# Optimization experiments

Measured on AMD Instinct MI355X. Metric: run time of the kernel, lower is better.

The kernel has to match this reference:

```python
import jax, jax.numpy as jnp
import numpy as np

B, E, F, Q = 16, 2048, 8192, 20
D, WD = 256, 300
NUM_ENTITY, NUM_WORD, NUM_RELATION = 100000, 50000, 600
NUM_LAYER = 3
PAGERANK_LAMBDA = 0.8
FACT_SCALE = 3.0
VERY_NEG = -100000000000.0
VERY_SMALL = 1e-10


def setup_inputs() -> dict:
    key = jax.random.key(0)
    ks = jax.random.split(key, 40)
    s = 0.05
    L = NUM_LAYER
    inp = {
        'local_entity': jax.random.randint(ks[0], (B, E), 0, NUM_ENTITY),
        'q2e_adj_mat': jax.random.uniform(ks[1], (B, E, 1), jnp.float32),
        'kb_fact_rel': jax.random.randint(ks[2], (B, F), 0, NUM_RELATION),
        'query_text': jax.random.randint(ks[3], (B, Q), 0, NUM_WORD),
        'answer_dist': jax.random.uniform(ks[4], (B, E), jnp.float32),
        'e2f_ent': jax.random.randint(ks[5], (B, F), 0, E),
        'f2e_ent': jax.random.randint(ks[6], (B, F), 0, E),
        'word_emb': jax.random.normal(ks[7], (NUM_WORD + 1, WD)) * s,
        'entity_emb': jax.random.normal(ks[8], (NUM_ENTITY + 1, WD)) * s,
        'relation_emb': jax.random.normal(ks[9], (NUM_RELATION + 1, 2 * WD)) * s,
        'entity_lin_w': jax.random.normal(ks[10], (D, WD)) * s,
        'entity_lin_b': jnp.zeros((D,)),
        'relation_lin_w': jax.random.normal(ks[11], (D, 2 * WD)) * s,
        'relation_lin_b': jnp.zeros((D,)),
        'lstm_w_ih': jax.random.normal(ks[12], (4 * D, WD)) * s,
        'lstm_w_hh': jax.random.normal(ks[13], (4 * D, D)) * s,
        'lstm_b_ih': jnp.zeros((4 * D,)),
        'lstm_b_hh': jnp.zeros((4 * D,)),
        'q2e_w': jax.random.normal(ks[14], (L, D, D)) * s,
        'q2e_b': jnp.zeros((L, D)),
        'e2q_w': jax.random.normal(ks[15], (L, D, 3 * D)) * s,
        'e2q_b': jnp.zeros((L, D)),
        'e2e_w': jax.random.normal(ks[16], (L, D, 3 * D)) * s,
        'e2e_b': jnp.zeros((L, D)),
        'kb_head_w': jax.random.normal(ks[17], (L, D, D)) * s,
        'kb_head_b': jnp.zeros((L, D)),
        'kb_tail_w': jax.random.normal(ks[18], (L, D, D)) * s,
        'kb_tail_b': jnp.zeros((L, D)),
        'kb_self_w': jax.random.normal(ks[19], (L, D, D)) * s,
        'kb_self_b': jnp.zeros((L, D)),
        'score_w': jax.random.normal(ks[20], (1, D)) * s,
        'score_b': jnp.zeros((1,)),
    }
    return inp


def _lstm(x, w_ih, w_hh, b_ih, b_hh):
    # torch LSTM, single layer, unidirectional, zero init state; gates (i,f,g,o)
    gx = jnp.einsum('btd,gd->btg', x, w_ih) + b_ih + b_hh  # [B,T,4H]
    H = w_hh.shape[1]
    init = (jnp.zeros((x.shape[0], H), x.dtype), jnp.zeros((x.shape[0], H), x.dtype))
    def step(carry, g):
        h, c = carry
        z = g + h @ w_hh.T
        i, f, gg, o = jnp.split(z, 4, axis=-1)
        c = jax.nn.sigmoid(f) * c + jax.nn.sigmoid(i) * jnp.tanh(gg)
        h = jax.nn.sigmoid(o) * jnp.tanh(c)
        return (h, c), h
    (h, _), hs = jax.lax.scan(step, init, jnp.swapaxes(gx, 0, 1))
    return jnp.swapaxes(hs, 0, 1), h  # [B,T,H], [B,H]


def _forward(local_entity, q2e_adj_mat, kb_fact_rel, query_text, e2f_ent, f2e_ent,
             word_emb, entity_emb, relation_emb,
             entity_lin_w, entity_lin_b, relation_lin_w, relation_lin_b,
             lstm_w_ih, lstm_w_hh, lstm_b_ih, lstm_b_hh,
             q2e_w, q2e_b, e2q_w, e2q_b, e2e_w, e2e_b,
             kb_head_w, kb_head_b, kb_tail_w, kb_tail_b, kb_self_w, kb_self_b,
             score_w, score_b):
    bidx = jnp.arange(B)[:, None]
    ent_mask = (local_entity != NUM_ENTITY).astype(jnp.float32)  # [B,E]
    q_mask = (query_text != NUM_WORD).astype(jnp.float32)        # [B,Q]

    # query LSTM encoding (dropout = identity in eval)
    qh, qlast = _lstm(word_emb[query_text], lstm_w_ih, lstm_w_hh, lstm_b_ih, lstm_b_hh)
    query_node = qlast[:, None, :]                               # [B,1,D]

    # fact embeddings
    lf = relation_emb[kb_fact_rel] @ relation_lin_w.T + relation_lin_b  # [B,F,D]
    div = jnp.sqrt(jnp.float32(D))

    # fact <-> query attention
    sim = jnp.einsum('bqd,bfd->bqf', qh, lf) / div
    sim = jax.nn.softmax(sim + (1.0 - q_mask)[:, :, None] * VERY_NEG, axis=1)
    att = jnp.einsum('bqf,bqd->bfd', sim, qh)
    Wf = jnp.sum(att * lf, axis=2) / div                          # [B,F]
    W_tilde = jnp.exp(Wf - jnp.max(Wf, axis=1, keepdims=True))    # [B,F]

    # e2f softmax normalizer: scatter-add fact weights onto head entities
    e2f_softmax = jnp.zeros((B, E), W_tilde.dtype).at[bidx, e2f_ent].add(W_tilde)
    e2f_softmax = jnp.maximum(e2f_softmax, VERY_SMALL)

    # entity embeddings (word_dim != entity_dim -> linear projection)
    le = entity_emb[local_entity] @ entity_lin_w.T + entity_lin_b  # [B,E,D]
    pagerank = q2e_adj_mat[..., 0]                                 # [B,E]

    for i in range(NUM_LAYER):
        q2e = jnp.broadcast_to(query_node @ q2e_w[i].T + q2e_b[i], (B, E, D))
        # fact update: self + gathered head-entity messages
        fact_self = lf @ kb_self_w[i].T + kb_self_b[i]
        head = le @ kb_head_w[i].T + kb_head_b[i]
        e2f_emb = jax.nn.relu(fact_self + jnp.take_along_axis(head, e2f_ent[:, :, None], axis=1))
        norm = W_tilde * jnp.take_along_axis(pagerank / e2f_softmax, e2f_ent, axis=1)  # [B,F]
        e2f_emb = e2f_emb * norm[:, :, None]
        # entity update: self + scattered tail messages
        tail = e2f_emb @ kb_tail_w[i].T + kb_tail_b[i]
        ent_self = le @ kb_self_w[i].T + kb_self_b[i]
        f2e_emb = jax.nn.relu(ent_self + jnp.zeros((B, E, D), le.dtype).at[bidx, f2e_ent].add(tail))
        pagerank = (PAGERANK_LAMBDA * jnp.zeros((B, E), norm.dtype).at[bidx, f2e_ent].add(norm)
                    + (1.0 - PAGERANK_LAMBDA) * pagerank)
        nxt = jnp.concatenate([le, q2e, FACT_SCALE * f2e_emb], axis=2)  # [B,E,3D]
        query_node = jnp.einsum('be,bed->bd', pagerank, nxt @ e2q_w[i].T + e2q_b[i])[:, None, :]
        le = jax.nn.relu(nxt @ e2e_w[i].T + e2e_b[i])

    score = (le @ score_w.T + score_b)[..., 0]                     # [B,E]
    return score


def reference(local_entity, q2e_adj_mat, kb_fact_rel, query_text, answer_dist,
              e2f_ent, f2e_ent, word_emb, entity_emb, relation_emb,
              entity_lin_w, entity_lin_b, relation_lin_w, relation_lin_b,
              lstm_w_ih, lstm_w_hh, lstm_b_ih, lstm_b_hh,
              q2e_w, q2e_b, e2q_w, e2q_b, e2e_w, e2e_b,
              kb_head_w, kb_head_b, kb_tail_w, kb_tail_b, kb_self_w, kb_self_b,
              score_w, score_b):
    return _forward(local_entity, q2e_adj_mat, kb_fact_rel, query_text, e2f_ent, f2e_ent,
                    word_emb, entity_emb, relation_emb,
                    entity_lin_w, entity_lin_b, relation_lin_w, relation_lin_b,
                    lstm_w_ih, lstm_w_hh, lstm_b_ih, lstm_b_hh,
                    q2e_w, q2e_b, e2q_w, e2q_b, e2e_w, e2e_b,
                    kb_head_w, kb_head_b, kb_tail_w, kb_tail_b, kb_self_w, kb_self_b,
                    score_w, score_b)
```

## Files before the change

kernel.cpp:

```cpp
#include <hip/hip_runtime.h>
#include <hip/hip_bf16.h>

typedef __hip_bfloat16 bf16;
typedef __attribute__((ext_vector_type(8))) short bf16x8;
typedef __attribute__((ext_vector_type(4))) float f32x4;

#define BB 16
#define EE 2048
#define FF 8192
#define QQ 20
#define DD 256
#define WDIM 300
#define NWORD 50000
#define VERY_NEG_F (-1.0e11f)

static __device__ __forceinline__ float b2f(bf16 x){ return __bfloat162float(x); }
static __device__ __forceinline__ bf16 f2b(float x){ return __float2bfloat16(x); }
static __device__ __forceinline__ float sigm(float x){ return 1.f/(1.f+expf(-x)); }
static __device__ __forceinline__ void ld4bf(const bf16* p, float v[4]){
  short4 s = *(const short4*)p;
  v[0]=b2f(*(const bf16*)&s.x); v[1]=b2f(*(const bf16*)&s.y);
  v[2]=b2f(*(const bf16*)&s.z); v[3]=b2f(*(const bf16*)&s.w);
}
static __device__ __forceinline__ void st4bf(bf16* p, float a,float b,float c,float d){
  unsigned short u[4]; bf16 t;
  t=f2b(a);u[0]=*(unsigned short*)&t; t=f2b(b);u[1]=*(unsigned short*)&t;
  t=f2b(c);u[2]=*(unsigned short*)&t; t=f2b(d);u[3]=*(unsigned short*)&t;
  *(short4*)p=*(short4*)u;
}

#define O_GX       0UL
#define O_QH       1310720UL
#define O_QNODE    1638400UL
#define O_RELLIN   1654784UL
#define O_WR       2270208UL
#define O_WMAX     2308864UL
#define O_WT       2309120UL
#define O_E2FS     2833408UL
#define O_PR       2964480UL
#define O_PRAGG    3095552UL
#define O_Q2EV     3226624UL
#define O_Q2EVB    3243008UL
#define O_RELSELF  3251200UL
#define O_NORM     3866624UL
#define O_WNXT     4390912UL
#define O_PRSUM    4440064UL
#define O_CNT      4440320UL
#define O_CUR      4571392UL
#define O_BSTART   4702464UL
#define O_BIDX     4834048UL
#define O_ELWPAD   5358336UL
#define O_FLAG     5522176UL
#define O_CVT      5522432UL
#define O_AGG      10915584UL
#define O_ENTSELF  27692800UL
#define O_LEA      44470016UL
#define O_LEB      61247232UL
#define O_HEAD     78024448UL
#define O_F2EEMB   94801664UL

#define C_ELB   0
#define C_RLW   256
#define C_RLB   153856
#define C_WIH   154112
#define C_WHH   461312
#define C_BIH   723456
#define C_BHH   724480
#define C_Q2EW  725504
#define C_Q2EB  922112
#define C_E2QW  922880
#define C_E2QB  1512704
#define C_E2EW  1513472
#define C_E2EB  2103296
#define C_KHW   2104064
#define C_KHB   2300672
#define C_KTW   2301440
#define C_KTB   2498048
#define C_KSW   2498816
#define C_KSB   2695424
#define C_SCW   2696192
#define C_SCB   2696448

__global__ __launch_bounds__(256) void k_sniff(const unsigned short* ee, int* flag){
  __shared__ int red[256];
  int c=0;
  for(int i=threadIdx.x;i<4096;i+=256){
    int ex=(ee[2*i]>>7)&0xFF;
    c += (ex>=192);
  }
  red[threadIdx.x]=c; __syncthreads();
  for(int o=128;o;o>>=1){ if(threadIdx.x<o) red[threadIdx.x]+=red[threadIdx.x+o]; __syncthreads(); }
  if(!threadIdx.x) flag[0] = (red[0]>64) ? 1 : 0;
}

struct CvtJobs{ const void* src[20]; bf16* dst[20]; int n[20]; int sc[20]; };
__global__ __launch_bounds__(256) void k_cvt(CvtJobs J, const int* dfl){
  const int isf=*dfl;
  int j=blockIdx.y;
  int n=J.n[j];
  int i4=(blockIdx.x*256+threadIdx.x)*4;
  if(i4>=n) return;
  float m = (J.sc[j] && ((i4%768)>=512)) ? 3.f : 1.f;
  bf16* d=J.dst[j]+i4;
  if(isf){
    const float* s=(const float*)J.src[j]+i4;
    if(i4+4<=n){ float4 t=*(const float4*)s; st4bf(d,t.x*m,t.y*m,t.z*m,t.w*m); }
    else for(int r=0;i4+r<n;r++) d[r]=f2b(s[r]*m);
  } else {
    const bf16* s=(const bf16*)J.src[j]+i4;
    if(i4+4<=n){ float v[4]; ld4bf(s,v); st4bf(d,v[0]*m,v[1]*m,v[2]*m,v[3]*m); }
    else for(int r=0;i4+r<n;r++) d[r]=f2b(b2f(s[r])*m);
  }
}

__global__ __launch_bounds__(256) void k_cvtwhh(const void* src, bf16* wf, const int* dfl){
  const int isf=*dfl;
  int fid=blockIdx.x*256+threadIdx.x;
  int lane=fid&63, kt=(fid>>6)&7, gt=fid>>9;
  int l16=lane&15, q=lane>>4;
  long so=(long)(gt*16+l16)*256 + kt*32 + q*8;
  float v[8];
  if(isf){ const float* s=(const float*)src+so;
    #pragma unroll
    for(int j=0;j<8;j++) v[j]=s[j];
  } else { const bf16* s=(const bf16*)src+so; ld4bf(s,v); ld4bf(s+4,v+4); }
  bf16* d=wf+(long)fid*8;
  st4bf(d,v[0],v[1],v[2],v[3]); st4bf(d+4,v[4],v[5],v[6],v[7]);
}

__global__ __launch_bounds__(256) void k_cvtelw(const void* src, bf16* dst, const int* dfl){
  const int isf=*dfl;
  int r=blockIdx.x;
  for(int c=threadIdx.x;c<320;c+=256){
    float v=0.f;
    if(c<300) v = isf ? ((const float*)src)[r*300+c] : b2f(((const bf16*)src)[r*300+c]);
    dst[(long)r*320+c]=f2b(v);
  }
}

__global__ __launch_bounds__(256) void k_cnt(const int* f2e, int* cnt){
  int i=blockIdx.x*256+threadIdx.x;
  atomicAdd(&cnt[((i>>13)<<11)+f2e[i]], 1);
}
__global__ __launch_bounds__(1024) void k_scan(const int* cnt, int* bstart){
  __shared__ int ps[1024];
  int t=threadIdx.x;
  int loc[32]; int s=0;
  #pragma unroll
  for(int j=0;j<32;j++){ loc[j]=s; s+=cnt[t*32+j]; }
  ps[t]=s; __syncthreads();
  for(int off=1;off<1024;off<<=1){
    int v=(t>=off)?ps[t-off]:0;
    __syncthreads(); ps[t]+=v; __syncthreads();
  }
  int base=(t? ps[t-1]:0);
  #pragma unroll
  for(int j=0;j<32;j++) bstart[t*32+j]=base+loc[j];
  if(t==1023) bstart[32768]=ps[1023];
}
__global__ __launch_bounds__(256) void k_fill(const int* f2e, const int* bstart, int* cur, int* bidx){
  int i=blockIdx.x*256+threadIdx.x;
  int key=((i>>13)<<11)+f2e[i];
  int pos=bstart[key]+atomicAdd(&cur[key],1);
  bidx[pos]=i;
}

__global__ __launch_bounds__(256) void k_gx(const int* qtext, const void* wemb,
    const bf16* wih, const bf16* bih, const bf16* bhh, float* gx, const int* dfl,
    int* lcnt){
  if(blockIdx.x==0 && threadIdx.x<32) lcnt[threadIdx.x]=0;
  const int isf=*dfl;
  int bt=blockIdx.x;
  __shared__ float xr[WDIM];
  int w=qtext[bt];
  for(int k4=threadIdx.x*4;k4<WDIM;k4+=1024){
    if(isf){ float4 t=*(const float4*)((const float*)wemb+(long)w*WDIM+k4);
             xr[k4]=t.x;xr[k4+1]=t.y;xr[k4+2]=t.z;xr[k4+3]=t.w; }
    else   { float v[4]; ld4bf((const bf16*)wemb+(long)w*WDIM+k4,v);
             xr[k4]=v[0];xr[k4+1]=v[1];xr[k4+2]=v[2];xr[k4+3]=v[3]; }
  }
  __syncthreads();
  #pragma unroll
  for(int s=0;s<4;s++){
    int g=threadIdx.x+256*s;
    float acc=b2f(bih[g])+b2f(bhh[g]);
    const bf16* wr=wih+(long)g*WDIM;
    for(int k4=0;k4<WDIM;k4+=4){
      float v[4]; ld4bf(wr+k4,v);
      acc+=v[0]*xr[k4]+v[1]*xr[k4+1]+v[2]*xr[k4+2]+v[3]*xr[k4+3];
    }
    gx[bt*1024+g]=acc;
  }
}

#define NLB 8
__global__ __launch_bounds__(512) void k_mega(const float* gx, const bf16* wf,
    float* qh, float* qnode, bf16* hbuf, int* lcnt,
    const void* remb, const bf16* rlw, const bf16* rlb, float* rel_lin,
    const int* local_entity, const void* emb, bf16* A0,
    const void* adj, float* pr, const int* dfl){
  const int bid=blockIdx.x, tid=threadIdx.x;
  if(bid<NLB){
    __shared__ bf16  hlds[16*264];
    __shared__ float zs[4*16*32];
    __shared__ bf16  hsl[512];
    const int k=bid;
    const int wv=tid>>6, lane=tid&63, q=lane>>4, l16=lane&15;
    const int gt=(wv>>1)*16 + k*2 + (wv&1);
    const int b=tid>>5, u=tid&31, gu=k*32+u;
    bf16x8 wreg[8];
    #pragma unroll
    for(int kt=0;kt<8;kt++)
      wreg[kt]=*(const bf16x8*)(wf + (((long)(gt*8+kt))*64 + lane)*8);
    float c=0.f;
    float gxr[4];
    #pragma unroll
    for(int g=0;g<4;g++) gxr[g]=gx[(b*QQ+0)*1024 + g*256 + gu];
    for(int t=0;t<QQ;t++){
      f32x4 acc=(f32x4){0.f,0.f,0.f,0.f};
      if(t){
        while(__hip_atomic_load(lcnt+(t-1), __ATOMIC_RELAXED, __HIP_MEMORY_SCOPE_AGENT) < NLB)
          __builtin_amdgcn_s_sleep(2);
        __builtin_amdgcn_sched_barrier(0);
        const bf16* hb = hbuf + (t&1)*4096;
        {
          int r=tid>>5, cc=(tid&31)*8;
          unsigned long long v0=__hip_atomic_load((const unsigned long long*)(hb + r*256 + cc),
                         __ATOMIC_RELAXED, __HIP_MEMORY_SCOPE_AGENT);
          unsigned long long v1=__hip_atomic_load((const unsigned long long*)(hb + r*256 + cc + 4),
                         __ATOMIC_RELAXED, __HIP_MEMORY_SCOPE_AGENT);
          *(unsigned long long*)&hlds[r*264 + cc] = v0;
          *(unsigned long long*)&hlds[r*264 + cc + 4] = v1;
        }
        __syncthreads();
        #pragma unroll
        for(int kt=0;kt<8;kt++){
          bf16x8 af=*(const bf16x8*)&hlds[l16*264 + kt*32 + q*8];
          acc=__builtin_amdgcn_mfma_f32_16x16x32_bf16(af,wreg[kt],acc,0,0,0);
        }
      }
      #pragma unroll
      for(int r=0;r<4;r++) zs[(wv>>1)*512 + (q*4+r)*32 + (wv&1)*16 + l16]=acc[r];
      __syncthreads();
      float zi=zs[0*512+b*32+u]+gxr[0];
      float zf=zs[1*512+b*32+u]+gxr[1];
      float zg=zs[2*512+b*32+u]+gxr[2];
      float zo=zs[3*512+b*32+u]+gxr[3];
      { int tn=(t<QQ-1)?t+1:t;
        #pragma unroll
        for(int g=0;g<4;g++) gxr[g]=gx[(b*QQ+tn)*1024 + g*256 + gu];
      }
      c=sigm(zf)*c+sigm(zi)*tanhf(zg);
      float hv=sigm(zo)*tanhf(c);
      hsl[tid]=f2b(hv);
      __syncthreads();
      if(t<QQ-1){
        if(tid<128){
          bf16* hw=hbuf + ((t+1)&1)*4096;
          int bb=tid>>3, p=tid&7;
          unsigned long long v=*(unsigned long long*)&hsl[bb*32+p*4];
          __hip_atomic_store((unsigned long long*)(hw + bb*256 + k*32 + p*4), v,
                             __ATOMIC_RELAXED, __HIP_MEMORY_SCOPE_AGENT);
        }
        __syncthreads();
        if(tid==0)
          __hip_atomic_fetch_add(lcnt+t, 1, __ATOMIC_RELAXED, __HIP_MEMORY_SCOPE_AGENT);
      }
      __builtin_nontemporal_store(hv, &qh[(long)(b*QQ+t)*256+gu]);
      if(t==QQ-1) qnode[(b<<8)+gu]=hv;
    }
  } else if(bid<309){
    __shared__ float rr[2][2*WDIM];
    const int isf=*dfl;
    const int half=tid>>8, d=tid&255;
    const int r=(bid-8)*2+half;
    if(r<601){
      for(int k4=d*4;k4<2*WDIM;k4+=1024){
        if(isf){ float4 t4=*(const float4*)((const float*)remb+(long)r*2*WDIM+k4);
                 rr[half][k4]=t4.x;rr[half][k4+1]=t4.y;rr[half][k4+2]=t4.z;rr[half][k4+3]=t4.w; }
        else   { float v[4]; ld4bf((const bf16*)remb+(long)r*2*WDIM+k4,v);
                 rr[half][k4]=v[0];rr[half][k4+1]=v[1];rr[half][k4+2]=v[2];rr[half][k4+3]=v[3]; }
      }
    }
    __syncthreads();
    if(r<601){
      float acc=b2f(rlb[d]);
      const bf16* wr=rlw+(long)d*2*WDIM;
      for(int k4=0;k4<2*WDIM;k4+=4){
        float v[4]; ld4bf(wr+k4,v);
        acc+=v[0]*rr[half][k4]+v[1]*rr[half][k4+1]+v[2]*rr[half][k4+2]+v[3]*rr[half][k4+3];
      }
      rel_lin[r*DD+d]=acc;
    }
  } else if(bid<325){
    const int isf=*dfl;
    int i4=((bid-309)*512+tid)*4;
    if(isf){ *(float4*)(pr+i4)=*(const float4*)((const float*)adj+i4); }
    else { float v[4]; ld4bf((const bf16*)adj+i4,v);
           float4 t; t.x=v[0];t.y=v[1];t.z=v[2];t.w=v[3]; *(float4*)(pr+i4)=t; }
  } else {
    const int isf=*dfl;
    int row=(bid-325)*4+(tid>>7); int t=tid&127;
    int ent=local_entity[row];
    bf16* dst=A0+(long)row*320;
    if(t<75){
      float v[4];
      if(isf){ float4 x=*(const float4*)((const float*)emb+(long)ent*WDIM+t*4);
               v[0]=x.x;v[1]=x.y;v[2]=x.z;v[3]=x.w; }
      else ld4bf((const bf16*)emb+(long)ent*WDIM+t*4, v);
      st4bf(dst+t*4, v[0],v[1],v[2],v[3]);
    } else if(t<80){
      st4bf(dst+t*4, 0.f,0.f,0.f,0.f);
    }
  }
}

__global__ __launch_bounds__(256) void k_simwr(const float* qh, const float* rel_lin,
    const int* qtext, float* Wr){
  int b = blockIdx.x, rc = blockIdx.y;
  __shared__ float qhb[QQ*DD];
  __shared__ float qm[QQ];
  for(int i=threadIdx.x;i<QQ*DD;i+=256) qhb[i]=qh[b*QQ*DD+i];
  if(threadIdx.x<QQ) qm[threadIdx.x] = (qtext[b*QQ+threadIdx.x]!=NWORD)?0.f:VERY_NEG_F;
  __syncthreads();
  int r = rc*256+threadIdx.x;
  if(r>=601) return;
  float s[QQ];
  #pragma unroll
  for(int q=0;q<QQ;q++) s[q]=0.f;
  for(int k=0;k<DD;k++){
    float rl = rel_lin[r*DD+k];
    #pragma unroll
    for(int q=0;q<QQ;q++) s[q] += qhb[q*DD+k]*rl;
  }
  float m=-1e30f;
  #pragma unroll
  for(int q=0;q<QQ;q++){ s[q]*=0.0625f; m=fmaxf(m, s[q]+qm[q]); }
  float sum=0.f, w=0.f;
  #pragma unroll
  for(int q=0;q<QQ;q++){ float p=expf(s[q]+qm[q]-m); sum+=p; w+=p*s[q]; }
  Wr[b*601+r] = w/sum;
}

__global__ __launch_bounds__(256) void k_wmax(const float* Wr, const int* rel, float* wmax,
    float* e2fs){
  int b=blockIdx.x; __shared__ float red[256];
  {
    int g=b*256+threadIdx.x;
    float4 z={0.f,0.f,0.f,0.f};
    *(float4*)(e2fs+g*8)=z; *(float4*)(e2fs+g*8+4)=z;
  }
  float m=-1e30f;
  for(int f=threadIdx.x;f<FF;f+=256) m=fmaxf(m, Wr[b*601+rel[b*FF+f]]);
  red[threadIdx.x]=m; __syncthreads();
  for(int o=128;o;o>>=1){ if(threadIdx.x<o) red[threadIdx.x]=fmaxf(red[threadIdx.x],red[threadIdx.x+o]); __syncthreads(); }
  if(!threadIdx.x) wmax[b]=red[0];
}
__global__ __launch_bounds__(256) void k_wt(const float* Wr, const int* rel,
    const float* wmax, const int* e2f, float* wt, float* e2fs,
    float* pragg, float* wnxtb, float* prsum){
  int i = blockIdx.x*256+threadIdx.x;
  if(i<32768) pragg[i]=0.f;
  if(i<12288) wnxtb[i]=0.f;
  if(i<16)    prsum[i]=0.f;
  int b = i>>13;
  float v = expf(Wr[b*601+rel[i]] - wmax[b]);
  wt[i]=v;
  atomicAdd(e2fs + (b<<11) + e2f[i], v);
}

template<int TK,int CONCAT,int EPI>
static __device__ __forceinline__ void mg_body(const bf16* A, const bf16* W,
    const bf16* bias, bf16* out, const bf16* Aq2, const bf16* Af2,
    const int* cnt, const bf16* addb, int m0, int tid){
  const int lane=tid&63, q=lane>>4, l16=lane&15;
  const int n0=(tid>>6)*64;
  const int bidx_=m0>>11;
  f32x4 acc[4][4];
  #pragma unroll
  for(int i=0;i<4;i++)
    #pragma unroll
    for(int j=0;j<4;j++) acc[i][j]=(f32x4){0.f,0.f,0.f,0.f};
  #pragma unroll
  for(int k0=0;k0<TK;k0+=32){
    int kk=k0+q*8;
    bf16x8 af[4], bw[4];
    #pragma unroll
    for(int mi=0;mi<4;mi++){
      int row=m0+mi*16+l16;
      const bf16* ap;
      if(CONCAT){
        if(kk<256)      ap=A  +(long)row*256+kk;
        else if(kk<512) ap=Aq2+(bidx_<<8)+(kk-256);
        else            ap=Af2+(long)row*256+(kk-512);
      } else ap=A+(long)row*TK+kk;
      af[mi]=*(const bf16x8*)ap;
    }
    #pragma unroll
    for(int ni=0;ni<4;ni++)
      bw[ni]=*(const bf16x8*)(W+(long)(n0+ni*16+l16)*TK+kk);
    #pragma unroll
    for(int mi=0;mi<4;mi++)
      #pragma unroll
      for(int ni=0;ni<4;ni++)
        acc[mi][ni]=__builtin_amdgcn_mfma_f32_16x16x32_bf16(af[mi],bw[ni],acc[mi][ni],0,0,0);
  }
  #pragma unroll
  for(int ni=0;ni<4;ni++){
    int col=n0+ni*16+l16;
    float bv=b2f(bias[col]);
    #pragma unroll
    for(int mi=0;mi<4;mi++){
      #pragma unroll
      for(int r=0;r<4;r++){
        int row=m0+mi*16+q*4+r;
        float v=acc[mi][ni][r];
        if(EPI==0) v+=bv;
        else if(EPI==1) v=fmaxf(v+bv,0.f);
        else {
          v += (float)cnt[row]*bv + b2f(addb[(long)row*256+col]);
          v=fmaxf(v,0.f);
        }
        out[(long)row*256+col]=f2b(v);
      }
    }
  }
}

struct MG {
  const bf16* A; const bf16* W; const bf16* bias; bf16* out;
  const bf16* Aq2; const bf16* Af2;
  const int* cnt; const bf16* addb;
};
template<int CONCAT,int EPI,int TK>
__global__ __launch_bounds__(256) void k_mgemm(MG p){
  mg_body<TK,CONCAT,EPI>(p.A,p.W,p.bias,p.out,p.Aq2,p.Af2,p.cnt,p.addb,
                         blockIdx.x*64,threadIdx.x);
}

struct L1 {
  const float* rel_lin; const bf16* ksw; const bf16* ksb;
  const float* qnode; const bf16* q2ew; const bf16* q2eb;
  float* relself; float* q2ev; bf16* q2evb;
  const bf16* A; const bf16* khw; const bf16* khb; bf16* headb; bf16* entself;
  const float* wt; const float* pr; const float* e2fs;
  const int* e2f; const int* f2e; float* normv; float* pragg;
};
__global__ __launch_bounds__(256) void k_lay1(L1 p){
  const int bid=blockIdx.x, tid=threadIdx.x;
  if(bid<617){
    __shared__ float xr[DD];
    int d=tid;
    if(bid<601){
      xr[d]=p.rel_lin[bid*DD+d]; __syncthreads();
      float acc=b2f(p.ksb[d]);
      const bf16* wr=p.ksw+(long)d*DD;
      for(int k4=0;k4<DD;k4+=4){
        float v[4]; ld4bf(wr+k4,v);
        acc+=v[0]*xr[k4]+v[1]*xr[k4+1]+v[2]*xr[k4+2]+v[3]*xr[k4+3];
      }
      p.relself[bid*DD+d]=acc;
    } else {
      int b=bid-601;
      xr[d]=p.qnode[(b<<8)+d]; __syncthreads();
      float acc=b2f(p.q2eb[d]);
      const bf16* wr=p.q2ew+(long)d*DD;
      for(int k4=0;k4<DD;k4+=4){
        float v[4]; ld4bf(wr+k4,v);
        acc+=v[0]*xr[k4]+v[1]*xr[k4+1]+v[2]*xr[k4+2]+v[3]*xr[k4+3];
      }
      p.q2ev[(b<<8)+d]=acc;
      p.q2evb[(b<<8)+d]=f2b(acc);
    }
  } else if(bid<1641){
    int g=bid-617;
    int m0=(g&511)*64;
    if(g<512) mg_body<256,0,0>(p.A,p.khw,p.khb,p.headb,0,0,0,0,m0,tid);
    else      mg_body<256,0,0>(p.A,p.ksw,p.ksb,p.entself,0,0,0,0,m0,tid);
  } else {
    int i=(bid-1641)*256+tid;
    int b=i>>13;
    int e=p.e2f[i];
    float v=p.wt[i]*p.pr[(b<<11)+e]/fmaxf(p.e2fs[(b<<11)+e],1e-10f);
    p.normv[i]=v;
    atomicAdd(p.pragg+(b<<11)+p.f2e[i], v);
  }
}

__global__ __launch_bounds__(256) void k_agg(const int* bstart, const int* bidx,
    const int* rel, const int* e2f, const float* normv, const float* relself,
    const bf16* head, bf16* agg){
  int eidx=blockIdx.x*4+(threadIdx.x>>6);
  int lane=threadIdx.x&63;
  int b=eidx>>11;
  float a0=0.f,a1=0.f,a2=0.f,a3=0.f;
  int s=bstart[eidx], e=bstart[eidx+1];
  for(int i=s;i<e;i++){
    int f=bidx[i];
    int r=rel[f]; int ent=e2f[f]; float nv=normv[f];
    float4 rs=*(const float4*)&relself[r*DD+lane*4];
    float hd[4]; ld4bf(head+(long)(((b<<11)+ent)*DD+lane*4),hd);
    a0+=fmaxf(rs.x+hd[0],0.f)*nv; a1+=fmaxf(rs.y+hd[1],0.f)*nv;
    a2+=fmaxf(rs.z+hd[2],0.f)*nv; a3+=fmaxf(rs.w+hd[3],0.f)*nv;
  }
  st4bf(agg+(long)eidx*DD+lane*4, a0,a1,a2,a3);
}

__global__ __launch_bounds__(256) void k_wnxt(const float* praggc, float* pragg, float* pr,
    const bf16* le, const bf16* f2e, float* wnxt, float* prsum){
  __shared__ float r1[4*256];
  __shared__ float r3[4*256];
  __shared__ float rp[4];
  const int b=blockIdx.x, ch=blockIdx.y;
  const int wv=threadIdx.x>>6, lane=threadIdx.x&63;
  const int pe0=(b<<11)+ch*64+wv*16;
  float pv=0.f;
  if(lane<16){
    int pe=pe0+lane;
    pv=0.8f*praggc[pe]+0.2f*pr[pe];
    pr[pe]=pv;
    pragg[pe]=0.f;
  }
  float a1[4]={0.f,0.f,0.f,0.f}, a3[4]={0.f,0.f,0.f,0.f}, ap=0.f;
  #pragma unroll
  for(int r=0;r<16;r++){
    float p=__shfl(pv, r, 64);
    long base=((long)(pe0+r))<<8;
    float v1[4],v3[4];
    ld4bf(le +base+lane*4, v1);
    ld4bf(f2e+base+lane*4, v3);
    #pragma unroll
    for(int j=0;j<4;j++){ a1[j]+=p*v1[j]; a3[j]+=p*v3[j]; }
    ap+=p;
  }
  #pragma unroll
  for(int j=0;j<4;j++){ r1[wv*256+lane*4+j]=a1[j]; r3[wv*256+lane*4+j]=a3[j]; }
  if(!lane) rp[wv]=ap;
  __syncthreads();
  const int t=threadIdx.x;
  float s1=r1[t]+r1[256+t]+r1[512+t]+r1[768+t];
  float s3=r3[t]+r3[256+t]+r3[512+t]+r3[768+t];
  atomicAdd(&wnxt[b*768+t], s1);
  atomicAdd(&wnxt[b*768+512+t], s3);
  if(!t) atomicAdd(&prsum[b], rp[0]+rp[1]+rp[2]+rp[3]);
}

__global__ __launch_bounds__(256) void k_e2eq(MG p, const float* q2ev,
    const bf16* qw, const bf16* qb, float* wnxtb, float* prsum, float* qnode){
  if(blockIdx.x<512){
    mg_body<768,1,1>(p.A,p.W,p.bias,p.out,p.Aq2,p.Af2,0,0,blockIdx.x*64,threadIdx.x);
  } else {
    int b=blockIdx.x-512, d=threadIdx.x;
    __shared__ float xr[768];
    float ps=prsum[b];
    xr[d]=wnxtb[b*768+d];            wnxtb[b*768+d]=0.f;
    xr[256+d]=ps*q2ev[(b<<8)+d];
    xr[512+d]=wnxtb[b*768+512+d];    wnxtb[b*768+512+d]=0.f;
    __syncthreads();
    if(d==0) prsum[b]=0.f;
    float acc=0.f;
    const bf16* wr=qw+(long)d*768;
    for(int k4=0;k4<768;k4+=4){
      float v[4]; ld4bf(wr+k4,v);
      acc+=v[0]*xr[k4]+v[1]*xr[k4+1]+v[2]*xr[k4+2]+v[3]*xr[k4+3];
    }
    qnode[(b<<8)+d]=acc+ps*b2f(qb[d]);
  }
}

__global__ __launch_bounds__(256) void k_score(const bf16* le, const bf16* sw,
    const bf16* sb, void* out, const int* dfl){
  const int isf=*dfl;
  int o=blockIdx.x*4 + (threadIdx.x>>6);
  int lane=threadIdx.x&63;
  float v[4],wv[4];
  ld4bf(le+(long)o*DD+lane*4,v); ld4bf(sw+lane*4,wv);
  float acc=v[0]*wv[0]+v[1]*wv[1]+v[2]*wv[2]+v[3]*wv[3];
  for(int off=32;off;off>>=1) acc+=__shfl_down(acc,off,64);
  if(!lane){
    float r=acc+b2f(sb[0]);
    if(isf) ((float*)out)[o]=r; else ((bf16*)out)[o]=f2b(r);
  }
}

extern "C" void kernel_launch(void* const* d_in, const int* in_sizes, int n_in,
                              void* d_out, int out_size, void* d_ws, size_t ws_size,
                              hipStream_t stream){
  const int*  local_entity=(const int*)d_in[0];
  const void* q2e_adj     =d_in[1];
  const int*  kb_fact_rel =(const int*)d_in[2];
  const int*  query_text  =(const int*)d_in[3];
  const int*  e2f_ent     =(const int*)d_in[5];
  const int*  f2e_ent     =(const int*)d_in[6];
  const void* word_emb    =d_in[7];
  const void* entity_emb  =d_in[8];
  const void* relation_emb=d_in[9];

  char* ws=(char*)d_ws;
  float* gx      =(float*)(ws+O_GX);
  float* qh      =(float*)(ws+O_QH);
  float* qnode   =(float*)(ws+O_QNODE);
  float* rel_lin =(float*)(ws+O_RELLIN);
  float* Wr      =(float*)(ws+O_WR);
  float* wmax    =(float*)(ws+O_WMAX);
  float* wt      =(float*)(ws+O_WT);
  float* e2fs    =(float*)(ws+O_E2FS);
  float* pr      =(float*)(ws+O_PR);
  float* pragg   =(float*)(ws+O_PRAGG);
  float* q2ev    =(float*)(ws+O_Q2EV);
  bf16*  q2evb   =(bf16*)(ws+O_Q2EVB);
  float* relself =(float*)(ws+O_RELSELF);
  float* normv   =(float*)(ws+O_NORM);
  float* wnxt    =(float*)(ws+O_WNXT);
  float* prsum   =(float*)(ws+O_PRSUM);
  int*   cnt     =(int*)(ws+O_CNT);
  int*   cur     =(int*)(ws+O_CUR);
  int*   bstart  =(int*)(ws+O_BSTART);
  int*   bidx    =(int*)(ws+O_BIDX);
  bf16*  elwpad  =(bf16*)(ws+O_ELWPAD);
  int*   dflag   =(int*)(ws+O_FLAG);
  bf16*  cw      =(bf16*)(ws+O_CVT);
  bf16*  agg     =(bf16*)(ws+O_AGG);
  bf16*  A0      =(bf16*)(ws+O_AGG);
  bf16*  entself =(bf16*)(ws+O_ENTSELF);
  bf16*  leA     =(bf16*)(ws+O_LEA);
  bf16*  leB     =(bf16*)(ws+O_LEB);
  bf16*  headb   =(bf16*)(ws+O_HEAD);
  bf16*  f2eemb  =(bf16*)(ws+O_F2EEMB);
  bf16*  hbuf    =(bf16*)(ws+O_LEA);
  int*   lcnt    =(int*)(ws+O_LEA+16384);

  k_sniff<<<1,256,0,stream>>>((const unsigned short*)entity_emb, dflag);

  CvtJobs J;
  int cntj=0;
  auto add=[&](int in_idx, long coff, int n, int sc){
    J.src[cntj]=d_in[in_idx]; J.dst[cntj]=cw+coff; J.n[cntj]=n; J.sc[cntj]=sc; cntj++;
  };
  add(11,C_ELB,256,0);
  add(12,C_RLW,153600,0);  add(13,C_RLB,256,0);
  add(14,C_WIH,307200,0);
  add(16,C_BIH,1024,0);    add(17,C_BHH,1024,0);
  add(18,C_Q2EW,196608,0); add(19,C_Q2EB,768,0);
  add(20,C_E2QW,589824,1); add(21,C_E2QB,768,0);
  add(22,C_E2EW,589824,1); add(23,C_E2EB,768,0);
  add(24,C_KHW,196608,0);  add(25,C_KHB,768,0);
  add(26,C_KTW,196608,0);  add(27,C_KTB,768,0);
  add(28,C_KSW,196608,0);  add(29,C_KSB,768,0);
  add(30,C_SCW,256,0);     add(31,C_SCB,1,0);
  k_cvt<<<dim3(576,20),256,0,stream>>>(J, dflag);
  k_cvtwhh<<<128,256,0,stream>>>(d_in[15], cw+C_WHH, dflag);
  k_cvtelw<<<256,256,0,stream>>>(d_in[10], elwpad, dflag);

  hipMemsetAsync(cnt, 0, (size_t)2*BB*EE*4, stream);
  k_cnt <<<BB*FF/256,256,0,stream>>>(f2e_ent, cnt);
  k_scan<<<1,1024,0,stream>>>(cnt, bstart);
  k_fill<<<BB*FF/256,256,0,stream>>>(f2e_ent, bstart, cur, bidx);

  k_gx   <<<BB*QQ,256,0,stream>>>(query_text, word_emb, cw+C_WIH, cw+C_BIH, cw+C_BHH, gx, dflag, lcnt);
  k_mega<<<8517,512,0,stream>>>(gx, cw+C_WHH, qh, qnode, hbuf, lcnt,
      relation_emb, cw+C_RLW, cw+C_RLB, rel_lin,
      local_entity, entity_emb, A0,
      q2e_adj, pr, dflag);
  k_simwr<<<dim3(BB,3),256,0,stream>>>(qh, rel_lin, query_text, Wr);
  k_wmax <<<BB,256,0,stream>>>(Wr, kb_fact_rel, wmax, e2fs);
  k_wt   <<<BB*FF/256,256,0,stream>>>(Wr, kb_fact_rel, wmax, e2f_ent, wt, e2fs,
                                      pragg, wnxt, prsum);

  {
    MG p{}; p.A=A0; p.W=elwpad; p.bias=cw+C_ELB; p.out=leA;
    k_mgemm<0,0,320><<<BB*EE/64,256,0,stream>>>(p);
  }

  bf16* le_cur=leA; bf16* le_nxt=leB;
  for(int i=0;i<3;i++){
    {
      L1 p{};
      p.rel_lin=rel_lin; p.ksw=cw+C_KSW+(long)i*65536; p.ksb=cw+C_KSB+(long)i*256;
      p.qnode=qnode; p.q2ew=cw+C_Q2EW+(long)i*65536; p.q2eb=cw+C_Q2EB+(long)i*256;
      p.relself=relself; p.q2ev=q2ev; p.q2evb=q2evb;
      p.A=le_cur; p.khw=cw+C_KHW+(long)i*65536; p.khb=cw+C_KHB+(long)i*256;
      p.headb=headb; p.entself=entself;
      p.wt=wt; p.pr=pr; p.e2fs=e2fs;
      p.e2f=e2f_ent; p.f2e=f2e_ent; p.normv=normv; p.pragg=pragg;
      k_lay1<<<2153,256,0,stream>>>(p);
    }
    k_agg <<<BB*EE/4,256,0,stream>>>(bstart, bidx, kb_fact_rel, e2f_ent, normv, relself, headb, agg);
    {
      MG p{}; p.A=agg; p.W=cw+C_KTW+(long)i*65536; p.bias=cw+C_KTB+(long)i*256;
      p.out=f2eemb; p.cnt=cnt; p.addb=entself;
      k_mgemm<0,2,256><<<BB*EE/64,256,0,stream>>>(p);
    }
    k_wnxt <<<dim3(BB,32),256,0,stream>>>(pragg, pragg, pr, le_cur, f2eemb, wnxt, prsum);
    {
      MG p{}; p.A=le_cur; p.W=cw+C_E2EW+(long)i*196608; p.bias=cw+C_E2EB+(long)i*256;
      p.out=le_nxt; p.Aq2=q2evb; p.Af2=f2eemb;
      k_e2eq<<<512+BB,256,0,stream>>>(p, q2ev,
          cw+C_E2QW+(long)i*196608, cw+C_E2QB+(long)i*256, wnxt, prsum, qnode);
    }
    bf16* t=le_cur; le_cur=le_nxt; le_nxt=t;
  }

  k_score<<<BB*EE/4,256,0,stream>>>(le_cur, cw+C_SCW, cw+C_SCB, d_out, dflag);
}
```

Before: 979.2 us.

## Stage GEMM A tiles into LDS via async global_load_lds with 128-row blocks

Rewrites the layer GEMMs (kb_head/kb_self, kb_tail, e2e) to use 512-thread blocks that cover 128 rows. Each block stages its 128x256 bf16 A tile into swizzled LDS with global_load_lds, and the warps then read fragments from LDS. The head and self GEMMs now share one staged tile, and the e2e concat GEMM stages both A operands and broadcasts the per-batch query fragment directly. The aim is to cut redundant global loads of A and improve reuse, at the cost of 64-128KB of LDS per block, which lowers occupancy. The e2e blocks also have to hold two 64KB buffers.

```diff
diff --git a/kernel.cpp b/kernel.cpp
--- a/kernel.cpp
+++ b/kernel.cpp
@@ -4,6 +4,8 @@
 typedef __hip_bfloat16 bf16;
 typedef __attribute__((ext_vector_type(8))) short bf16x8;
 typedef __attribute__((ext_vector_type(4))) float f32x4;
+typedef __attribute__((address_space(1))) const void* gas_t;
+typedef __attribute__((address_space(3))) void* las_t;
 
 #define BB 16
 #define EE 2048
@@ -345,8 +347,7 @@
 __global__ __launch_bounds__(256) void k_wmax(const float* Wr, const int* rel, float* wmax,
     float* e2fs){
   int b=blockIdx.x; __shared__ float red[256];
-  {
-    int g=b*256+threadIdx.x;
+  { int g=b*256+threadIdx.x;
     float4 z={0.f,0.f,0.f,0.f};
     *(float4*)(e2fs+g*8)=z; *(float4*)(e2fs+g*8+4)=z;
   }
@@ -369,13 +370,17 @@
   atomicAdd(e2fs + (b<<11) + e2f[i], v);
 }
 
-template<int TK,int CONCAT,int EPI>
-static __device__ __forceinline__ void mg_body(const bf16* A, const bf16* W,
-    const bf16* bias, bf16* out, const bf16* Aq2, const bf16* Af2,
-    const int* cnt, const bf16* addb, int m0, int tid){
-  const int lane=tid&63, q=lane>>4, l16=lane&15;
-  const int n0=(tid>>6)*64;
-  const int bidx_=m0>>11;
+struct MG {
+  const bf16* A; const bf16* W; const bf16* bias; bf16* out;
+  const bf16* Aq2; const bf16* Af2;
+  const int* cnt; const bf16* addb;
+};
+template<int CONCAT,int EPI,int TK>
+__global__ __launch_bounds__(256) void k_mgemm(MG p){
+  const int m0 = blockIdx.x*64;
+  const int lane = threadIdx.x&63;
+  const int q = lane>>4, l16 = lane&15;
+  const int n0 = (threadIdx.x>>6)*64;
   f32x4 acc[4][4];
   #pragma unroll
   for(int i=0;i<4;i++)
@@ -386,19 +391,65 @@
     int kk=k0+q*8;
     bf16x8 af[4], bw[4];
     #pragma unroll
+    for(int mi=0;mi<4;mi++)
+      af[mi]=*(const bf16x8*)(p.A+(long)(m0+mi*16+l16)*TK+kk);
+    #pragma unroll
+    for(int ni=0;ni<4;ni++)
+      bw[ni]=*(const bf16x8*)(p.W+(long)(n0+ni*16+l16)*TK+kk);
+    #pragma unroll
+    for(int mi=0;mi<4;mi++)
+      #pragma unroll
+      for(int ni=0;ni<4;ni++)
+        acc[mi][ni]=__builtin_amdgcn_mfma_f32_16x16x32_bf16(af[mi],bw[ni],acc[mi][ni],0,0,0);
+  }
+  #pragma unroll
+  for(int ni=0;ni<4;ni++){
+    int col=n0+ni*16+l16;
+    float bv=b2f(p.bias[col]);
+    #pragma unroll
     for(int mi=0;mi<4;mi++){
-      int row=m0+mi*16+l16;
-      const bf16* ap;
-      if(CONCAT){
-        if(kk<256)      ap=A  +(long)row*256+kk;
-        else if(kk<512) ap=Aq2+(bidx_<<8)+(kk-256);
-        else            ap=Af2+(long)row*256+(kk-512);
-      } else ap=A+(long)row*TK+kk;
-      af[mi]=*(const bf16x8*)ap;
-    }
-    #pragma unroll
-    for(int ni=0;ni<4;ni++)
-      bw[ni]=*(const bf16x8*)(W+(long)(n0+ni*16+l16)*TK+kk);
+      #pragma unroll
+      for(int r=0;r<4;r++){
+        int row=m0+mi*16+q*4+r;
+        float v=acc[mi][ni][r]+bv;
+        p.out[(long)row*256+col]=f2b(v);
+      }
+    }
+  }
+}
+
+static __device__ __forceinline__ void stage64(const char* g, char* l, int tid){
+  const int wv=tid>>6, lane=tid&63;
+  #pragma unroll
+  for(int it=0;it<8;++it){
+    int chunk=it*8192+wv*1024;
+    int off=chunk+lane*16;
+    int src=off^(((off>>9)&7)<<4);
+    __builtin_amdgcn_global_load_lds((gas_t)(g+src),(las_t)(l+chunk),16,0,0);
+  }
+}
+static __device__ __forceinline__ bf16x8 lds_a(const char* l, int r, int kk){
+  int b=(r*512+kk*2)^((r&7)<<4);
+  return *(const bf16x8*)(l+b);
+}
+template<int EPI>
+static __device__ __forceinline__ void mg2_k256(const char* ldsA, const bf16* W,
+    const bf16* bias, bf16* out, const int* cnt, const bf16* addb, int m0, int tid){
+  const int lane=tid&63, q=lane>>4, l16=lane&15;
+  const int wv=tid>>6, wr=wv>>2, wc=wv&3, n0=wc*64;
+  f32x4 acc[4][4];
+  #pragma unroll
+  for(int i=0;i<4;i++)
+    #pragma unroll
+    for(int j=0;j<4;j++) acc[i][j]=(f32x4){0.f,0.f,0.f,0.f};
+  #pragma unroll
+  for(int k0=0;k0<256;k0+=32){
+    int kk=k0+q*8;
+    bf16x8 af[4], bw[4];
+    #pragma unroll
+    for(int mi=0;mi<4;mi++) af[mi]=lds_a(ldsA, wr*64+mi*16+l16, kk);
+    #pragma unroll
+    for(int ni=0;ni<4;ni++) bw[ni]=*(const bf16x8*)(W+(long)(n0+ni*16+l16)*256+kk);
     #pragma unroll
     for(int mi=0;mi<4;mi++)
       #pragma unroll
@@ -413,7 +464,7 @@
     for(int mi=0;mi<4;mi++){
       #pragma unroll
       for(int r=0;r<4;r++){
-        int row=m0+mi*16+q*4+r;
+        int row=m0+wr*64+mi*16+q*4+r;
         float v=acc[mi][ni][r];
         if(EPI==0) v+=bv;
         else if(EPI==1) v=fmaxf(v+bv,0.f);
@@ -427,17 +478,6 @@
   }
 }
 
-struct MG {
-  const bf16* A; const bf16* W; const bf16* bias; bf16* out;
-  const bf16* Aq2; const bf16* Af2;
-  const int* cnt; const bf16* addb;
-};
-template<int CONCAT,int EPI,int TK>
-__global__ __launch_bounds__(256) void k_mgemm(MG p){
-  mg_body<TK,CONCAT,EPI>(p.A,p.W,p.bias,p.out,p.Aq2,p.Af2,p.cnt,p.addb,
-                         blockIdx.x*64,threadIdx.x);
-}
-
 struct L1 {
   const float* rel_lin; const bf16* ksw; const bf16* ksb;
   const float* qnode; const bf16* q2ew; const bf16* q2eb;
@@ -446,45 +486,60 @@
   const float* wt; const float* pr; const float* e2fs;
   const int* e2f; const int* f2e; float* normv; float* pragg;
 };
-__global__ __launch_bounds__(256) void k_lay1(L1 p){
+__global__ __launch_bounds__(512) void k_lay1(L1 p){
+  __shared__ char smem[65536];
   const int bid=blockIdx.x, tid=threadIdx.x;
   if(bid<617){
-    __shared__ float xr[DD];
-    int d=tid;
-    if(bid<601){
-      xr[d]=p.rel_lin[bid*DD+d]; __syncthreads();
-      float acc=b2f(p.ksb[d]);
-      const bf16* wr=p.ksw+(long)d*DD;
-      for(int k4=0;k4<DD;k4+=4){
-        float v[4]; ld4bf(wr+k4,v);
-        acc+=v[0]*xr[k4]+v[1]*xr[k4+1]+v[2]*xr[k4+2]+v[3]*xr[k4+3];
-      }
-      p.relself[bid*DD+d]=acc;
-    } else {
-      int b=bid-601;
-      xr[d]=p.qnode[(b<<8)+d]; __syncthreads();
-      float acc=b2f(p.q2eb[d]);
-      const bf16* wr=p.q2ew+(long)d*DD;
-      for(int k4=0;k4<DD;k4+=4){
-        float v[4]; ld4bf(wr+k4,v);
-        acc+=v[0]*xr[k4]+v[1]*xr[k4+1]+v[2]*xr[k4+2]+v[3]*xr[k4+3];
-      }
-      p.q2ev[(b<<8)+d]=acc;
-      p.q2evb[(b<<8)+d]=f2b(acc);
-    }
-  } else if(bid<1641){
-    int g=bid-617;
-    int m0=(g&511)*64;
-    if(g<512) mg_body<256,0,0>(p.A,p.khw,p.khb,p.headb,0,0,0,0,m0,tid);
-    else      mg_body<256,0,0>(p.A,p.ksw,p.ksb,p.entself,0,0,0,0,m0,tid);
+    float* xr=(float*)smem;
+    if(tid<256){
+      if(bid<601) xr[tid]=p.rel_lin[bid*DD+tid];
+      else        xr[tid]=p.qnode[((bid-601)<<8)+tid];
+    }
+    __syncthreads();
+    if(tid<256){
+      int d=tid;
+      if(bid<601){
+        float acc=b2f(p.ksb[d]);
+        const bf16* wr=p.ksw+(long)d*DD;
+        for(int k4=0;k4<DD;k4+=4){
+          float v[4]; ld4bf(wr+k4,v);
+          acc+=v[0]*xr[k4]+v[1]*xr[k4+1]+v[2]*xr[k4+2]+v[3]*xr[k4+3];
+        }
+        p.relself[bid*DD+d]=acc;
+      } else {
+        int b=bid-601;
+        float acc=b2f(p.q2eb[d]);
+        const bf16* wr=p.q2ew+(long)d*DD;
+        for(int k4=0;k4<DD;k4+=4){
+          float v[4]; ld4bf(wr+k4,v);
+          acc+=v[0]*xr[k4]+v[1]*xr[k4+1]+v[2]*xr[k4+2]+v[3]*xr[k4+3];
+        }
+        p.q2ev[(b<<8)+d]=acc;
+        p.q2evb[(b<<8)+d]=f2b(acc);
+      }
+    }
+  } else if(bid<873){
+    int m0=(bid-617)*128;
+    stage64((const char*)(p.A+(long)m0*256), smem, tid);
+    __syncthreads();
+    mg2_k256<0>(smem, p.khw, p.khb, p.headb, 0, 0, m0, tid);
+    mg2_k256<0>(smem, p.ksw, p.ksb, p.entself, 0, 0, m0, tid);
   } else {
-    int i=(bid-1641)*256+tid;
+    int i=(bid-873)*512+tid;
     int b=i>>13;
     int e=p.e2f[i];
     float v=p.wt[i]*p.pr[(b<<11)+e]/fmaxf(p.e2fs[(b<<11)+e],1e-10f);
     p.normv[i]=v;
     atomicAdd(p.pragg+(b<<11)+p.f2e[i], v);
   }
+}
+
+__global__ __launch_bounds__(512) void k_ktg(MG p){
+  __shared__ char smem[65536];
+  int m0=blockIdx.x*128;
+  stage64((const char*)(p.A+(long)m0*256), smem, threadIdx.x);
+  __syncthreads();
+  mg2_k256<2>(smem, p.W, p.bias, p.out, p.cnt, p.addb, m0, threadIdx.x);
 }
 
 __global__ __launch_bounds__(256) void k_agg(const int* bstart, const int* bidx,
@@ -545,26 +600,100 @@
   if(!t) atomicAdd(&prsum[b], rp[0]+rp[1]+rp[2]+rp[3]);
 }
 
-__global__ __launch_bounds__(256) void k_e2eq(MG p, const float* q2ev,
+__global__ __launch_bounds__(512) void k_e2eq(MG p, const float* q2ev,
     const bf16* qw, const bf16* qb, float* wnxtb, float* prsum, float* qnode){
-  if(blockIdx.x<512){
-    mg_body<768,1,1>(p.A,p.W,p.bias,p.out,p.Aq2,p.Af2,0,0,blockIdx.x*64,threadIdx.x);
+  __shared__ char sA[65536];
+  __shared__ char sF[65536];
+  const int tid=threadIdx.x;
+  if(blockIdx.x<256){
+    int m0=blockIdx.x*128;
+    stage64((const char*)(p.A  +(long)m0*256), sA, tid);
+    stage64((const char*)(p.Af2+(long)m0*256), sF, tid);
+    __syncthreads();
+    const int lane=tid&63, q=lane>>4, l16=lane&15;
+    const int wv=tid>>6, wr=wv>>2, wc=wv&3, n0=wc*64;
+    const bf16* aq2 = p.Aq2 + ((m0>>11)<<8);
+    f32x4 acc[4][4];
+    #pragma unroll
+    for(int i=0;i<4;i++)
+      #pragma unroll
+      for(int j=0;j<4;j++) acc[i][j]=(f32x4){0.f,0.f,0.f,0.f};
+    #pragma unroll
+    for(int k0=0;k0<256;k0+=32){
+      int kk=k0+q*8;
+      bf16x8 af[4], bw[4];
+      #pragma unroll
+      for(int mi=0;mi<4;mi++) af[mi]=lds_a(sA, wr*64+mi*16+l16, kk);
+      #pragma unroll
+      for(int ni=0;ni<4;ni++) bw[ni]=*(const bf16x8*)(p.W+(long)(n0+ni*16+l16)*768+kk);
+      #pragma unroll
+      for(int mi=0;mi<4;mi++)
+        #pragma unroll
+        for(int ni=0;ni<4;ni++)
+          acc[mi][ni]=__builtin_amdgcn_mfma_f32_16x16x32_bf16(af[mi],bw[ni],acc[mi][ni],0,0,0);
+    }
+    #pragma unroll
+    for(int k0=256;k0<512;k0+=32){
+      int kk=k0+q*8;
+      bf16x8 aq=*(const bf16x8*)(aq2+(kk-256));
+      bf16x8 bw[4];
+      #pragma unroll
+      for(int ni=0;ni<4;ni++) bw[ni]=*(const bf16x8*)(p.W+(long)(n0+ni*16+l16)*768+kk);
+      #pragma unroll
+      for(int mi=0;mi<4;mi++)
+        #pragma unroll
+        for(int ni=0;ni<4;ni++)
+          acc[mi][ni]=__builtin_amdgcn_mfma_f32_16x16x32_bf16(aq,bw[ni],acc[mi][ni],0,0,0);
+    }
+    #pragma unroll
+    for(int k0=512;k0<768;k0+=32){
+      int kk=k0+q*8;
+      bf16x8 af[4], bw[4];
+      #pragma unroll
+      for(int mi=0;mi<4;mi++) af[mi]=lds_a(sF, wr*64+mi*16+l16, kk-512);
+      #pragma unroll
+      for(int ni=0;ni<4;ni++) bw[ni]=*(const bf16x8*)(p.W+(long)(n0+ni*16+l16)*768+kk);
+      #pragma unroll
+      for(int mi=0;mi<4;mi++)
+        #pragma unroll
+        for(int ni=0;ni<4;ni++)
+          acc[mi][ni]=__builtin_amdgcn_mfma_f32_16x16x32_bf16(af[mi],bw[ni],acc[mi][ni],0,0,0);
+    }
+    #pragma unroll
+    for(int ni=0;ni<4;ni++){
+      int col=n0+ni*16+l16;
+      float bv=b2f(p.bias[col]);
+      #pragma unroll
+      for(int mi=0;mi<4;mi++){
+        #pragma unroll
+        for(int r=0;r<4;r++){
+          int row=m0+wr*64+mi*16+q*4+r;
+          p.out[(long)row*256+col]=f2b(fmaxf(acc[mi][ni][r]+bv,0.f));
+        }
+      }
+    }
   } else {
-    int b=blockIdx.x-512, d=threadIdx.x;
-    __shared__ float xr[768];
+    int b=blockIdx.x-256;
+    float* xr=(float*)sA;
     float ps=prsum[b];
-    xr[d]=wnxtb[b*768+d];            wnxtb[b*768+d]=0.f;
-    xr[256+d]=ps*q2ev[(b<<8)+d];
-    xr[512+d]=wnxtb[b*768+512+d];    wnxtb[b*768+512+d]=0.f;
+    if(tid<256){
+      int d=tid;
+      xr[d]=wnxtb[b*768+d];            wnxtb[b*768+d]=0.f;
+      xr[256+d]=ps*q2ev[(b<<8)+d];
+      xr[512+d]=wnxtb[b*768+512+d];    wnxtb[b*768+512+d]=0.f;
+    }
     __syncthreads();
-    if(d==0) prsum[b]=0.f;
-    float acc=0.f;
-    const bf16* wr=qw+(long)d*768;
-    for(int k4=0;k4<768;k4+=4){
-      float v[4]; ld4bf(wr+k4,v);
-      acc+=v[0]*xr[k4]+v[1]*xr[k4+1]+v[2]*xr[k4+2]+v[3]*xr[k4+3];
-    }
-    qnode[(b<<8)+d]=acc+ps*b2f(qb[d]);
+    if(tid<256){
+      int d=tid;
+      if(d==0) prsum[b]=0.f;
+      float acc=0.f;
+      const bf16* wr=qw+(long)d*768;
+      for(int k4=0;k4<768;k4+=4){
+        float v[4]; ld4bf(wr+k4,v);
+        acc+=v[0]*xr[k4]+v[1]*xr[k4+1]+v[2]*xr[k4+2]+v[3]*xr[k4+3];
+      }
+      qnode[(b<<8)+d]=acc+ps*b2f(qb[d]);
+    }
   }
 }
 
@@ -683,19 +812,19 @@
       p.headb=headb; p.entself=entself;
       p.wt=wt; p.pr=pr; p.e2fs=e2fs;
       p.e2f=e2f_ent; p.f2e=f2e_ent; p.normv=normv; p.pragg=pragg;
-      k_lay1<<<2153,256,0,stream>>>(p);
+      k_lay1<<<1129,512,0,stream>>>(p);
     }
     k_agg <<<BB*EE/4,256,0,stream>>>(bstart, bidx, kb_fact_rel, e2f_ent, normv, relself, headb, agg);
     {
       MG p{}; p.A=agg; p.W=cw+C_KTW+(long)i*65536; p.bias=cw+C_KTB+(long)i*256;
       p.out=f2eemb; p.cnt=cnt; p.addb=entself;
-      k_mgemm<0,2,256><<<BB*EE/64,256,0,stream>>>(p);
+      k_ktg<<<256,512,0,stream>>>(p);
     }
     k_wnxt <<<dim3(BB,32),256,0,stream>>>(pragg, pragg, pr, le_cur, f2eemb, wnxt, prsum);
     {
       MG p{}; p.A=le_cur; p.W=cw+C_E2EW+(long)i*196608; p.bias=cw+C_E2EB+(long)i*256;
       p.out=le_nxt; p.Aq2=q2evb; p.Af2=f2eemb;
-      k_e2eq<<<512+BB,256,0,stream>>>(p, q2ev,
+      k_e2eq<<<272,512,0,stream>>>(p, q2ev,
           cw+C_E2QW+(long)i*196608, cw+C_E2QB+(long)i*256, wnxt, prsum, qnode);
     }
     bf16* t=le_cur; le_cur=le_nxt; le_nxt=t;
```

After: 956.3 us. -2.3%, faster.
